# Kernel optimization log

Measured on AMD Instinct MI355X. Metric: run time of the kernel, lower is better.

Reference implementation:

```python
import jax, jax.numpy as jnp
import numpy as np

B, IN_BITS, NUM_LUTS, K = 1024, 4096, 16384, 6

def setup_inputs() -> dict:
    key = jax.random.key(0)
    k1, k2, k3 = jax.random.split(key, 3)
    x_bits = jax.random.uniform(k1, (B, IN_BITS), dtype=jnp.float32)
    table = jax.random.normal(k2, (NUM_LUTS, 2 ** K), dtype=jnp.float32) * 0.01
    conn_idx = jax.random.randint(k3, (NUM_LUTS, K), 0, IN_BITS, dtype=jnp.int64)
    return {"x_bits": x_bits, "table": table, "conn_idx": conn_idx}

def reference(x_bits, table, conn_idx):
    # threshold to binary bits: [B, IN_BITS]
    bits01 = (x_bits > 0.5)
    # gather connected bits per LUT: [B, NUM_LUTS, K]
    bits = bits01[:, conn_idx]
    # bit-pack (MSB first, matching idx = idx*2 + bit loop): [B, NUM_LUTS]
    powers = (2 ** jnp.arange(K - 1, -1, -1, dtype=jnp.int32))  # [K]
    idx = jnp.sum(bits.astype(jnp.int32) * powers, axis=-1)
    # per-LUT table lookup: table[l, idx[b, l]]
    lut_ids = jnp.arange(NUM_LUTS, dtype=jnp.int32)[None, :]  # [1, NUM_LUTS]
    out = table[lut_ids, idx]  # [B, NUM_LUTS]
    return jax.nn.sigmoid(out)
```

## Files before the change

### kernel.cpp

```cpp
#include <hip/hip_runtime.h>
#include <hip/hip_bf16.h>

constexpr int B        = 1024;
constexpr int IN_BITS  = 4096;
constexpr int NUM_LUTS = 16384;
constexpr int K        = 6;

constexpr int TPB        = 256;
constexpr int LUTS_PER_B = 256;
constexpr int CHUNKS     = 8;
constexpr int BCH        = B / CHUNKS;

__global__ __launch_bounds__(TPB) void pack_kernel(
    const float* __restrict__ x, unsigned* __restrict__ packedT)
{
    const int pos = blockIdx.x * TPB + threadIdx.x;
    const int g   = blockIdx.y;
    const float* xp = x + (size_t)g * 32 * IN_BITS + pos;
    unsigned word = 0;
#pragma unroll
    for (int j = 0; j < 32; ++j) {
        word |= (xp[(size_t)j * IN_BITS] > 0.5f) ? (1u << j) : 0u;
    }
    packedT[(size_t)g * IN_BITS + pos] = word;
}

__global__ __launch_bounds__(TPB, 2) void lut_kernel(
    const float*    __restrict__ table,
    const int*      __restrict__ conn,
    const unsigned* __restrict__ packedT,
    float*          __restrict__ out)
{
    __shared__ float tbl[LUTS_PER_B * 64];

    const int tid = threadIdx.x;
    const int l0  = blockIdx.x * LUTS_PER_B;
    const int l   = l0 + tid;

    {
        const float4* tsrc = (const float4*)(table + (size_t)l0 * 64);
        float4*       tdst = (float4*)tbl;
#pragma unroll
        for (int i = 0; i < 16; ++i) {
            tdst[tid + i * TPB] = tsrc[tid + i * TPB];
        }
    }

    int c[K];
#pragma unroll
    for (int k = 0; k < K; ++k) c[k] = conn[(size_t)l * K + k];

    __syncthreads();

    const int bbase = blockIdx.y * BCH;
    float* op = out + (size_t)bbase * NUM_LUTS + l;

    for (int g = 0; g < BCH / 32; ++g) {
        const unsigned* pr = packedT + (size_t)(bbase / 32 + g) * IN_BITS;
        unsigned w[K];
#pragma unroll
        for (int k = 0; k < K; ++k) w[k] = pr[c[k]];

#pragma unroll
        for (int j = 0; j < 32; ++j) {
            int idx = 0;
#pragma unroll
            for (int k = 0; k < K; ++k)
                idx = (idx << 1) | (int)((w[k] >> j) & 1u);
            float v = tbl[tid * 64 + idx];
            float s = 1.0f / (1.0f + __expf(-v));
            *op = s;
            op += NUM_LUTS;
        }
    }
}

extern "C" void kernel_launch(void* const* d_in, const int* in_sizes, int n_in,
                              void* d_out, int out_size, void* d_ws, size_t ws_size,
                              hipStream_t stream)
{
    const float* x_bits = (const float*)d_in[0];
    const float* table  = (const float*)d_in[1];
    const int*   conn   = (const int*)d_in[2];
    float* out = (float*)d_out;
    unsigned* packedT = (unsigned*)d_ws;

    dim3 g1(IN_BITS / TPB, B / 32);
    pack_kernel<<<g1, TPB, 0, stream>>>(x_bits, packedT);

    dim3 g2(NUM_LUTS / LUTS_PER_B, CHUNKS);
    lut_kernel<<<g2, TPB, 0, stream>>>(table, conn, packedT, out);
}
```

Before: 100.6 us.

## Precompute sigmoid of table transposed, remove LDS bank conflicts, nontemporal stores

The pack kernel and a new table pass are merged into one prep kernel. The table pass applies sigmoid once per table entry and writes the table transposed, entry-major, into workspace. The LUT kernel then reads its LDS table as [idx][lut], which avoids the stride-64 bank conflicts of the old [lut][idx] layout, and it drops the per-output exp. Output writes use nontemporal stores. The cost is one extra table read and write (4 MB each way) plus a larger workspace footprint.

```diff
diff --git a/kernel.cpp b/kernel.cpp
--- a/kernel.cpp
+++ b/kernel.cpp
@@ -11,38 +11,75 @@
 constexpr int CHUNKS     = 8;
 constexpr int BCH        = B / CHUNKS;
 
-__global__ __launch_bounds__(TPB) void pack_kernel(
-    const float* __restrict__ x, unsigned* __restrict__ packedT)
+constexpr int PACK_BLOCKS = (IN_BITS / TPB) * (B / 32);
+constexpr int TBL_BLOCKS  = NUM_LUTS / 64;
+
+__global__ __launch_bounds__(TPB) void prep_kernel(
+    const float* __restrict__ x, const float* __restrict__ table,
+    unsigned* __restrict__ packedT, float* __restrict__ tableT)
 {
-    const int pos = blockIdx.x * TPB + threadIdx.x;
-    const int g   = blockIdx.y;
-    const float* xp = x + (size_t)g * 32 * IN_BITS + pos;
-    unsigned word = 0;
+    __shared__ float tile[64][65];
+    const int tid = threadIdx.x;
+    const int blk = blockIdx.x;
+
+    if (blk < PACK_BLOCKS) {
+        const int pos = (blk % (IN_BITS / TPB)) * TPB + tid;
+        const int g   = blk / (IN_BITS / TPB);
+        const float* xp = x + (size_t)g * 32 * IN_BITS + pos;
+        unsigned word = 0;
 #pragma unroll
-    for (int j = 0; j < 32; ++j) {
-        word |= (xp[(size_t)j * IN_BITS] > 0.5f) ? (1u << j) : 0u;
+        for (int j = 0; j < 32; ++j)
+            word |= (xp[(size_t)j * IN_BITS] > 0.5f) ? (1u << j) : 0u;
+        packedT[(size_t)g * IN_BITS + pos] = word;
+    } else {
+        const int bt = blk - PACK_BLOCKS;
+        const int l0 = bt * 64;
+        const float4* src = (const float4*)(table + (size_t)l0 * 64);
+#pragma unroll
+        for (int i = 0; i < 4; ++i) {
+            int q = tid + i * 256;
+            float4 v = src[q];
+            int l = q >> 4;
+            int e = (q & 15) * 4;
+            tile[l][e + 0] = v.x; tile[l][e + 1] = v.y;
+            tile[l][e + 2] = v.z; tile[l][e + 3] = v.w;
+        }
+        __syncthreads();
+#pragma unroll
+        for (int i = 0; i < 4; ++i) {
+            int q  = tid + i * 256;
+            int e  = q >> 4;
+            int lc = (q & 15) * 4;
+            float4 v;
+            v.x = 1.0f / (1.0f + __expf(-tile[lc + 0][e]));
+            v.y = 1.0f / (1.0f + __expf(-tile[lc + 1][e]));
+            v.z = 1.0f / (1.0f + __expf(-tile[lc + 2][e]));
+            v.w = 1.0f / (1.0f + __expf(-tile[lc + 3][e]));
+            ((float4*)(tableT + (size_t)e * NUM_LUTS + l0))[q & 15] = v;
+        }
     }
-    packedT[(size_t)g * IN_BITS + pos] = word;
 }
 
 __global__ __launch_bounds__(TPB, 2) void lut_kernel(
-    const float*    __restrict__ table,
     const int*      __restrict__ conn,
     const unsigned* __restrict__ packedT,
+    const float*    __restrict__ tableT,
     float*          __restrict__ out)
 {
-    __shared__ float tbl[LUTS_PER_B * 64];
+    __shared__ float tbl[64 * LUTS_PER_B];
 
     const int tid = threadIdx.x;
     const int l0  = blockIdx.x * LUTS_PER_B;
     const int l   = l0 + tid;
 
     {
-        const float4* tsrc = (const float4*)(table + (size_t)l0 * 64);
-        float4*       tdst = (float4*)tbl;
+        float4* dst = (float4*)tbl;
 #pragma unroll
         for (int i = 0; i < 16; ++i) {
-            tdst[tid + i * TPB] = tsrc[tid + i * TPB];
+            int q = tid + i * 256;
+            int e = q >> 6;
+            int c = q & 63;
+            dst[q] = ((const float4*)(tableT + (size_t)e * NUM_LUTS + l0))[c];
         }
     }
 
@@ -67,9 +104,8 @@
 #pragma unroll
             for (int k = 0; k < K; ++k)
                 idx = (idx << 1) | (int)((w[k] >> j) & 1u);
-            float v = tbl[tid * 64 + idx];
-            float s = 1.0f / (1.0f + __expf(-v));
-            *op = s;
+            float v = tbl[idx * LUTS_PER_B + tid];
+            __builtin_nontemporal_store(v, op);
             op += NUM_LUTS;
         }
     }
@@ -83,11 +119,13 @@
     const float* table  = (const float*)d_in[1];
     const int*   conn   = (const int*)d_in[2];
     float* out = (float*)d_out;
+
     unsigned* packedT = (unsigned*)d_ws;
+    float*    tableT  = (float*)((char*)d_ws + 512 * 1024);
 
-    dim3 g1(IN_BITS / TPB, B / 32);
-    pack_kernel<<<g1, TPB, 0, stream>>>(x_bits, packedT);
+    prep_kernel<<<PACK_BLOCKS + TBL_BLOCKS, TPB, 0, stream>>>(
+        x_bits, table, packedT, tableT);
 
     dim3 g2(NUM_LUTS / LUTS_PER_B, CHUNKS);
-    lut_kernel<<<g2, TPB, 0, stream>>>(table, conn, packedT, out);
+    lut_kernel<<<g2, TPB, 0, stream>>>(conn, packedT, tableT, out);
 }
```

Result: faster. 94.88 us (-5.7%).
